# Performance work log

Measured on AMD Instinct MI355X. Metric: run time of the kernel, lower is better.

The kernel has to match this reference:

```python
import jax, jax.numpy as jnp
import numpy as np

THRESHOLD_FACTOR = 1.25


def setup_inputs() -> dict:
    key = jax.random.key(0)
    B, S, D = 2, 4096, 2
    r_embed = jax.random.normal(key, (B, S, D), dtype=jnp.float32)
    return {"r_embed": r_embed}


def reference(r_embed) -> jnp.ndarray:
    # r_embed: [B, S, 2]
    B, S, _ = r_embed.shape
    diff = r_embed[:, :, None, :] - r_embed[:, None, :, :]   # [B, S, S, 2]
    dx, dy = diff[..., 0], diff[..., 1]
    dist_sq = dx * dx + dy * dy                               # [B, S, S]
    # Safe atan2: at (0,0) (diagonal) atan2 returns 0 either way; the where
    # only guards against NaN gradients, forward value is identical.
    zero_pair = (dx == 0) & (dy == 0)
    phase_diff = jnp.arctan2(jnp.where(zero_pair, 0.0, dy),
                             jnp.where(zero_pair, 1.0, dx))
    forward_bias = 0.5 * (1.0 + jnp.cos(phase_diff))          # [B, S, S]
    mean_dist = jnp.mean(dist_sq, axis=(-1, -2), keepdims=True)
    # torch.std defaults to unbiased (ddof=1)
    std_dist = jnp.std(dist_sq, axis=(-1, -2), keepdims=True, ddof=1)
    threshold = mean_dist + THRESHOLD_FACTOR * std_dist
    causal_mask = jnp.tril(jnp.ones((S, S), dtype=bool))      # [S, S]
    valid_mask = (dist_sq <= threshold) & causal_mask[None]
    attention = valid_mask.astype(r_embed.dtype) * forward_bias
    return attention
```

## Files before the change

kernel.cpp:

```cpp
#include <hip/hip_runtime.h>
#include <math.h>

#define PAB_ROWS 16
#define PAB_TPB  256

__global__ __launch_bounds__(PAB_TPB) void pab_fused_kernel(
        const float* __restrict__ r, float* __restrict__ out, int S) {
    const int b = blockIdx.z;
    const float2* emb = (const float2*)r + (size_t)b * S;
    const int tid = threadIdx.x;

    double s[12];
#pragma unroll
    for (int k = 0; k < 12; ++k) s[k] = 0.0;

    for (int idx0 = tid * 4; idx0 < S; idx0 += PAB_TPB * 4) {
        float4 c0 = *(const float4*)(emb + idx0);
        float4 c1 = *(const float4*)(emb + idx0 + 2);
        float xs[4] = {c0.x, c0.z, c1.x, c1.z};
        float ys[4] = {c0.y, c0.w, c1.y, c1.w};
#pragma unroll
        for (int k = 0; k < 4; ++k) {
            if (idx0 + k >= S) break;
            double x = (double)xs[k], y = (double)ys[k];
            double x2 = x * x, y2 = y * y;
            s[0]  += x;        s[1]  += y;
            s[2]  += x2;       s[3]  += y2;
            s[4]  += x2 * x;   s[5]  += y2 * y;
            s[6]  += x2 * x2;  s[7]  += y2 * y2;
            s[8]  += x * y;    s[9]  += x2 * y;
            s[10] += x * y2;   s[11] += x2 * y2;
        }
    }

#pragma unroll
    for (int off = 32; off > 0; off >>= 1) {
#pragma unroll
        for (int k = 0; k < 12; ++k)
            s[k] += __shfl_down(s[k], off, 64);
    }

    __shared__ double part[PAB_TPB / 64][12];
    __shared__ double tot[12];
    __shared__ float thr_sh;
    const int wave = tid >> 6, lane = tid & 63;
    if (lane == 0) {
#pragma unroll
        for (int k = 0; k < 12; ++k) part[wave][k] = s[k];
    }
    __syncthreads();
    if (tid < 12) {
        double t = 0.0;
#pragma unroll
        for (int w = 0; w < PAB_TPB / 64; ++w) t += part[w][tid];
        tot[tid] = t;
    }
    __syncthreads();
    if (tid == 0) {
        double N = (double)S;
        double M = N * N;
        double S1x = tot[0], S1y = tot[1], S2x = tot[2], S2y = tot[3];
        double S3x = tot[4], S3y = tot[5], S4x = tot[6], S4y = tot[7];
        double A11 = tot[8], A21 = tot[9], A12 = tot[10], A22 = tot[11];

        double sum_d = 2.0 * N * (S2x + S2y) - 2.0 * (S1x * S1x + S1y * S1y);
        double qx = 2.0 * N * S4x - 8.0 * S3x * S1x + 6.0 * S2x * S2x;
        double qy = 2.0 * N * S4y - 8.0 * S3y * S1y + 6.0 * S2y * S2y;
        double cross = 2.0 * N * A22 - 4.0 * A21 * S1y - 4.0 * A12 * S1x
                     + 2.0 * S2x * S2y + 4.0 * A11 * A11;
        double sum_d2 = qx + qy + 2.0 * cross;

        double mean = sum_d / M;
        double var  = (sum_d2 - sum_d * sum_d / M) / (M - 1.0);
        thr_sh = (float)(mean + 1.25 * sqrt(var));
    }
    __syncthreads();
    const float thr = thr_sh;

    const int i0 = blockIdx.y * PAB_ROWS;
    const int jt0 = blockIdx.x * PAB_TPB * 4;
    const int j0 = jt0 + tid * 4;
    if (j0 >= S) return;

    size_t orow = ((size_t)b * S + i0) * S + j0;

    if (jt0 > i0 + PAB_ROWS - 1) {
        const float4 z = {0.0f, 0.0f, 0.0f, 0.0f};
#pragma unroll
        for (int rr = 0; rr < PAB_ROWS; ++rr) {
            if (i0 + rr < S) *(float4*)(out + orow) = z;
            orow += S;
        }
        return;
    }

    float2 pis[PAB_ROWS];
#pragma unroll
    for (int rr = 0; rr < PAB_ROWS; ++rr)
        pis[rr] = emb[min(i0 + rr, S - 1)];

    float4 c0 = *(const float4*)(emb + j0);
    float4 c1 = *(const float4*)(emb + j0 + 2);
    const float xs[4] = {c0.x, c0.z, c1.x, c1.z};
    const float ys[4] = {c0.y, c0.w, c1.y, c1.w};

#pragma unroll
    for (int rr = 0; rr < PAB_ROWS; ++rr) {
        const int i = i0 + rr;
        if (i < S) {
            const float2 pi = pis[rr];
            float4 res;
            float* rp = &res.x;
#pragma unroll
            for (int k = 0; k < 4; ++k) {
                float dx = pi.x - xs[k];
                float dy = pi.y - ys[k];
                float d2 = fmaf(dx, dx, dy * dy);
                float bias = (d2 > 0.0f) ? fmaf(0.5f * dx, rsqrtf(d2), 0.5f)
                                         : 1.0f;
                bool valid = (d2 <= thr) & ((j0 + k) <= i);
                rp[k] = valid ? bias : 0.0f;
            }
            *(float4*)(out + orow) = res;
        }
        orow += S;
    }
}

extern "C" void kernel_launch(void* const* d_in, const int* in_sizes, int n_in,
                              void* d_out, int out_size, void* d_ws, size_t ws_size,
                              hipStream_t stream) {
    const float* r = (const float*)d_in[0];
    float* out = (float*)d_out;
    (void)d_ws; (void)ws_size;

    long in0 = in_sizes[0];
    int S = (int)((2L * (long)out_size) / in0);
    int B = (int)(in0 / (2L * S));

    dim3 block(PAB_TPB);
    dim3 grid((S + PAB_TPB * 4 - 1) / (PAB_TPB * 4),
              (S + PAB_ROWS - 1) / PAB_ROWS, B);
    pab_fused_kernel<<<grid, block, 0, stream>>>(r, out, S);
}
```

Before: 141.0 us.

## Assign full rows per block to cut redundant per-block threshold reductions

Adds a templated kernel in which each block covers 8 complete output rows across all column tiles, looping over up to four column passes. The global mean/std threshold reduction, which every block recomputes in double precision, therefore runs in half as many blocks. The fallback kernel now writes all-zero upper-triangle tiles before computing the threshold, so those blocks skip the reduction entirely. In exchange, each block holds more registers for the extra column passes, and the grid has fewer blocks.

```diff
diff --git a/kernel.cpp b/kernel.cpp
--- a/kernel.cpp
+++ b/kernel.cpp
@@ -1,15 +1,11 @@
 #include <hip/hip_runtime.h>
 #include <math.h>
 
-#define PAB_ROWS 16
+#define PAB_ROWS 8
 #define PAB_TPB  256
 
-__global__ __launch_bounds__(PAB_TPB) void pab_fused_kernel(
-        const float* __restrict__ r, float* __restrict__ out, int S) {
-    const int b = blockIdx.z;
-    const float2* emb = (const float2*)r + (size_t)b * S;
-    const int tid = threadIdx.x;
-
+__device__ __forceinline__ float pab_threshold(const float2* __restrict__ emb,
+                                               int S, int tid) {
     double s[12];
 #pragma unroll
     for (int k = 0; k < 12; ++k) s[k] = 0.0;
@@ -75,28 +71,101 @@
         thr_sh = (float)(mean + 1.25 * sqrt(var));
     }
     __syncthreads();
-    const float thr = thr_sh;
-
-    const int i0 = blockIdx.y * PAB_ROWS;
+    return thr_sh;
+}
+
+__device__ __forceinline__ float4 pab_compute4(float2 pi, const float* xs,
+        const float* ys, float thr, int i, int j0) {
+    float4 res;
+    float* rp = &res.x;
+#pragma unroll
+    for (int k = 0; k < 4; ++k) {
+        float dx = pi.x - xs[k];
+        float dy = pi.y - ys[k];
+        float d2 = fmaf(dx, dx, dy * dy);
+        float bias = (d2 > 0.0f) ? fmaf(0.5f * dx, rsqrtf(d2), 0.5f) : 1.0f;
+        bool valid = (d2 <= thr) & ((j0 + k) <= i);
+        rp[k] = valid ? bias : 0.0f;
+    }
+    return res;
+}
+
+template<int NPASS>
+__global__ __launch_bounds__(PAB_TPB) void pab_rows_kernel(
+        const float* __restrict__ r, float* __restrict__ out, int S) {
+    const int b = blockIdx.y;
+    const float2* emb = (const float2*)r + (size_t)b * S;
+    const int tid = threadIdx.x;
+    const int i0  = blockIdx.x * PAB_ROWS;
+
+    const float thr = pab_threshold(emb, S, tid);
+
+    float2 pis[PAB_ROWS];
+#pragma unroll
+    for (int rr = 0; rr < PAB_ROWS; ++rr)
+        pis[rr] = emb[min(i0 + rr, S - 1)];
+
+    float xs[NPASS][4], ys[NPASS][4];
+#pragma unroll
+    for (int p = 0; p < NPASS; ++p) {
+        const int j0 = p * (PAB_TPB * 4) + tid * 4;
+        float4 c0 = *(const float4*)(emb + j0);
+        float4 c1 = *(const float4*)(emb + j0 + 2);
+        xs[p][0] = c0.x; xs[p][1] = c0.z; xs[p][2] = c1.x; xs[p][3] = c1.z;
+        ys[p][0] = c0.y; ys[p][1] = c0.w; ys[p][2] = c1.y; ys[p][3] = c1.w;
+    }
+
+    const float4 z = {0.0f, 0.0f, 0.0f, 0.0f};
+#pragma unroll
+    for (int rr = 0; rr < PAB_ROWS; ++rr) {
+        const int i = i0 + rr;
+        if (i >= S) break;
+        const float2 pi = pis[rr];
+        float* op = out + ((size_t)b * S + i) * S + tid * 4;
+#pragma unroll
+        for (int p = 0; p < NPASS; ++p) {
+            const int jb = p * (PAB_TPB * 4);
+            float4 res;
+            if (jb > i) {
+                res = z;
+            } else {
+                res = pab_compute4(pi, xs[p], ys[p], thr, i, jb + tid * 4);
+            }
+            *(float4*)(op + (size_t)jb) = res;
+        }
+    }
+}
+
+#define PAB_ROWS_FB 16
+__global__ __launch_bounds__(PAB_TPB) void pab_fused_kernel_fb(
+        const float* __restrict__ r, float* __restrict__ out, int S) {
+    const int b = blockIdx.z;
+    const float2* emb = (const float2*)r + (size_t)b * S;
+    const int tid = threadIdx.x;
+
+    const int i0  = blockIdx.y * PAB_ROWS_FB;
     const int jt0 = blockIdx.x * PAB_TPB * 4;
-    const int j0 = jt0 + tid * 4;
+    const int j0  = jt0 + tid * 4;
+    size_t orow = ((size_t)b * S + i0) * S + j0;
+
+    if (jt0 > i0 + PAB_ROWS_FB - 1) {
+        if (j0 < S) {
+            const float4 zz = {0.0f, 0.0f, 0.0f, 0.0f};
+#pragma unroll
+            for (int rr = 0; rr < PAB_ROWS_FB; ++rr) {
+                if (i0 + rr < S) *(float4*)(out + orow) = zz;
+                orow += S;
+            }
+        }
+        return;
+    }
+
+    const float thr = pab_threshold(emb, S, tid);
     if (j0 >= S) return;
 
-    size_t orow = ((size_t)b * S + i0) * S + j0;
-
-    if (jt0 > i0 + PAB_ROWS - 1) {
-        const float4 z = {0.0f, 0.0f, 0.0f, 0.0f};
-#pragma unroll
-        for (int rr = 0; rr < PAB_ROWS; ++rr) {
-            if (i0 + rr < S) *(float4*)(out + orow) = z;
-            orow += S;
-        }
-        return;
-    }
-
-    float2 pis[PAB_ROWS];
-#pragma unroll
-    for (int rr = 0; rr < PAB_ROWS; ++rr)
+    float2 pis[PAB_ROWS_FB];
+#pragma unroll
+    for (int rr = 0; rr < PAB_ROWS_FB; ++rr)
         pis[rr] = emb[min(i0 + rr, S - 1)];
 
     float4 c0 = *(const float4*)(emb + j0);
@@ -105,24 +174,10 @@
     const float ys[4] = {c0.y, c0.w, c1.y, c1.w};
 
 #pragma unroll
-    for (int rr = 0; rr < PAB_ROWS; ++rr) {
+    for (int rr = 0; rr < PAB_ROWS_FB; ++rr) {
         const int i = i0 + rr;
-        if (i < S) {
-            const float2 pi = pis[rr];
-            float4 res;
-            float* rp = &res.x;
-#pragma unroll
-            for (int k = 0; k < 4; ++k) {
-                float dx = pi.x - xs[k];
-                float dy = pi.y - ys[k];
-                float d2 = fmaf(dx, dx, dy * dy);
-                float bias = (d2 > 0.0f) ? fmaf(0.5f * dx, rsqrtf(d2), 0.5f)
-                                         : 1.0f;
-                bool valid = (d2 <= thr) & ((j0 + k) <= i);
-                rp[k] = valid ? bias : 0.0f;
-            }
-            *(float4*)(out + orow) = res;
-        }
+        if (i < S)
+            *(float4*)(out + orow) = pab_compute4(pis[rr], xs, ys, thr, i, j0);
         orow += S;
     }
 }
@@ -139,7 +194,20 @@
     int B = (int)(in0 / (2L * S));
 
     dim3 block(PAB_TPB);
-    dim3 grid((S + PAB_TPB * 4 - 1) / (PAB_TPB * 4),
-              (S + PAB_ROWS - 1) / PAB_ROWS, B);
-    pab_fused_kernel<<<grid, block, 0, stream>>>(r, out, S);
-}
+    const int tile = PAB_TPB * 4;
+    const int npass = (S + tile - 1) / tile;
+
+    if (S % tile == 0 && S % PAB_ROWS == 0 && npass >= 1 && npass <= 4) {
+        dim3 grid(S / PAB_ROWS, B);
+        switch (npass) {
+        case 1: pab_rows_kernel<1><<<grid, block, 0, stream>>>(r, out, S); break;
+        case 2: pab_rows_kernel<2><<<grid, block, 0, stream>>>(r, out, S); break;
+        case 3: pab_rows_kernel<3><<<grid, block, 0, stream>>>(r, out, S); break;
+        default: pab_rows_kernel<4><<<grid, block, 0, stream>>>(r, out, S); break;
+        }
+    } else {
+        dim3 grid((S + tile - 1) / tile,
+                  (S + PAB_ROWS_FB - 1) / PAB_ROWS_FB, B);
+        pab_fused_kernel_fb<<<grid, block, 0, stream>>>(r, out, S);
+    }
+}
```

New measurement: 142.6 us. About the same (+1.1%).
